# Kernel tuning notes

Measured on AMD Instinct MI355X. Metric: run time of the kernel, lower is better.

## Reference

```python
import jax, jax.numpy as jnp
import numpy as np

D_MODEL = 512
NUM_HEADS = 8
DEPTH = D_MODEL // NUM_HEADS
BATCH = 2
SEQ = 2048
NEG_INF_SCALE = -1e9


def setup_inputs() -> dict:
    key = jax.random.key(0)
    ks = jax.random.split(key, 9)
    s = 0.02
    return {
        "v": jax.random.normal(ks[0], (BATCH, SEQ, D_MODEL), jnp.float32),
        "q": jax.random.normal(ks[1], (BATCH, SEQ, D_MODEL), jnp.float32),
        "k": jax.random.normal(ks[2], (BATCH, SEQ, D_MODEL), jnp.float32),
        "mask": jax.random.randint(ks[3], (BATCH, 1, SEQ, SEQ), 0, 2, jnp.int32),
        "wq_w": jax.random.normal(ks[4], (D_MODEL, D_MODEL), jnp.float32) * s,
        "wq_b": jnp.zeros((D_MODEL,), jnp.float32),
        "wk_w": jax.random.normal(ks[5], (D_MODEL, D_MODEL), jnp.float32) * s,
        "wk_b": jnp.zeros((D_MODEL,), jnp.float32),
        "wv_w": jax.random.normal(ks[6], (D_MODEL, D_MODEL), jnp.float32) * s,
        "wv_b": jnp.zeros((D_MODEL,), jnp.float32),
        "wo_w": jax.random.normal(ks[7], (D_MODEL, D_MODEL), jnp.float32) * s,
        "wo_b": jnp.zeros((D_MODEL,), jnp.float32),
    }


def _split_heads(x, b):
    # [b, s, d_model] -> [b, h, s, depth]
    return x.reshape(b, -1, NUM_HEADS, DEPTH).transpose(0, 2, 1, 3)


def reference(v, q, k, mask, wq_w, wq_b, wk_w, wk_b, wv_w, wv_b, wo_w, wo_b):
    b = q.shape[0]
    vv = _split_heads(v @ wv_w + wv_b, b)  # [b,h,s,d]
    kk = _split_heads(k @ wk_w + wk_b, b)
    qq = _split_heads(q @ wq_w + wq_b, b)
    # NOTE: the original code swaps q/k at the helper call site, so logits = K @ Q^T.
    logits = jnp.einsum("bhkd,bhqd->bhkq", kk, qq) / jnp.sqrt(jnp.float32(DEPTH))
    logits = logits + mask.astype(jnp.float32) * NEG_INF_SCALE
    attn = jax.nn.softmax(logits, axis=-1)  # softmax over the query axis (faithful quirk)
    # output = A^T @ V  -> [b,h,q,d]
    out = jnp.einsum("bhkq,bhkd->bhqd", attn, vv)
    concat = out.transpose(0, 2, 1, 3).reshape(b, -1, D_MODEL)
    return concat @ wo_w + wo_b, attn
```

## Files before the change

kernel.cpp:

```cpp
#include <hip/hip_runtime.h>

#define S 2048
#define DM 512
#define NH 8
#define HD 64
#define NB 2
#define BH (NB * NH)
#define MROWS (NB * S)
#define QW (S / 32)

typedef __bf16 bf16x8 __attribute__((ext_vector_type(8)));
typedef float f32x4 __attribute__((ext_vector_type(4)));

union FragU {
  uint4 u;
  bf16x8 v;
  unsigned short s[8];
};

__device__ __forceinline__ unsigned short f2bf(float x) {
  unsigned u = __float_as_uint(x);
  u += 0x7FFFu + ((u >> 16) & 1u);
  return (unsigned short)(u >> 16);
}

__global__ void k_wtrans(const float* __restrict__ w0, const float* __restrict__ w1,
                         const float* __restrict__ w2, const float* __restrict__ w3,
                         unsigned short* __restrict__ wt) {
  __shared__ float tile[64][65];
  int i = blockIdx.z;
  const float* w = (i == 0) ? w0 : (i == 1) ? w1 : (i == 2) ? w2 : w3;
  int k0 = blockIdx.x * 64;
  int n0 = blockIdx.y * 64;
  int tx = threadIdx.x, ty = threadIdx.y;
  for (int r = ty; r < 64; r += 4)
    tile[r][tx] = w[(size_t)(k0 + r) * DM + n0 + tx];
  __syncthreads();
  unsigned short* o = wt + (size_t)i * DM * DM;
  for (int r = ty; r < 64; r += 4)
    o[(size_t)(n0 + r) * DM + k0 + tx] = f2bf(tile[tx][r]);
}

__global__ __launch_bounds__(256) void k_cvt(
    const float* __restrict__ q, const float* __restrict__ k, const float* __restrict__ v,
    unsigned short* __restrict__ oq, unsigned short* __restrict__ ok, unsigned short* __restrict__ ov) {
  int which = blockIdx.y;
  const float* src = (which == 0) ? q : (which == 1) ? k : v;
  unsigned short* dst = (which == 0) ? oq : (which == 1) ? ok : ov;
  size_t t = (size_t)blockIdx.x * 256 + threadIdx.x;
  const float4* s4 = (const float4*)src + t * 2;
  float4 x = s4[0], y = s4[1];
  FragU f;
  f.s[0] = f2bf(x.x); f.s[1] = f2bf(x.y); f.s[2] = f2bf(x.z); f.s[3] = f2bf(x.w);
  f.s[4] = f2bf(y.x); f.s[5] = f2bf(y.y); f.s[6] = f2bf(y.z); f.s[7] = f2bf(y.w);
  *(uint4*)(dst + t * 8) = f.u;
}

__global__ __launch_bounds__(256) void k_maskpack(const int* __restrict__ mask,
                                                  unsigned* __restrict__ mp) {
  size_t gid = (size_t)blockIdx.x * 256 + threadIdx.x;
  int m = mask[gid];
  unsigned long long bal = __ballot(m != 0);
  int lane = threadIdx.x & 63;
  if (lane == 0) {
    uint2 wds = make_uint2((unsigned)bal, (unsigned)(bal >> 32));
    *(uint2*)&mp[gid >> 5] = wds;
  }
}

__global__ __launch_bounds__(256) void k_proj(
    const unsigned short* __restrict__ inq, const unsigned short* __restrict__ ink,
    const unsigned short* __restrict__ inv, const unsigned short* __restrict__ wt,
    const float* __restrict__ bq, const float* __restrict__ bk, const float* __restrict__ bv,
    unsigned short* __restrict__ oq, unsigned short* __restrict__ ok, unsigned short* __restrict__ ov) {
  int which = blockIdx.z;
  const unsigned short* in = (which == 0) ? inq : (which == 1) ? ink : inv;
  const float* bias = (which == 0) ? bq : (which == 1) ? bk : bv;
  unsigned short* out = (which == 0) ? oq : (which == 1) ? ok : ov;
  const unsigned short* w = wt + (size_t)which * DM * DM;

  int lane = threadIdx.x & 63, wv = threadIdx.x >> 6;
  int m0 = blockIdx.x * 64 + wv * 16;
  int n0 = blockIdx.y * 64;
  int kf = (lane >> 4) * 8;
  int arow = m0 + (lane & 15);

  f32x4 acc[4] = {{0.f, 0.f, 0.f, 0.f}, {0.f, 0.f, 0.f, 0.f},
                  {0.f, 0.f, 0.f, 0.f}, {0.f, 0.f, 0.f, 0.f}};

  for (int kk0 = 0; kk0 < DM; kk0 += 32) {
    FragU af;
    af.u = *(const uint4*)(in + (size_t)arow * DM + kk0 + kf);
#pragma unroll
    for (int nt = 0; nt < 4; nt++) {
      FragU bfr;
      bfr.u = *(const uint4*)(w + (size_t)(n0 + nt * 16 + (lane & 15)) * DM + kk0 + kf);
      acc[nt] = __builtin_amdgcn_mfma_f32_16x16x32_bf16(af.v, bfr.v, acc[nt], 0, 0, 0);
    }
  }
#pragma unroll
  for (int nt = 0; nt < 4; nt++) {
#pragma unroll
    for (int r = 0; r < 4; r++) {
      int row = m0 + (lane >> 4) * 4 + r;
      int col = n0 + nt * 16 + (lane & 15);
      float val = acc[nt][r] + bias[col];
      int b = row >> 11, sIdx = row & (S - 1);
      int h = col >> 6, d = col & 63;
      out[(((size_t)(b * NH + h) * S) + sIdx) * HD + d] = f2bf(val);
    }
  }
}

__global__ void k_vtrans(const unsigned short* __restrict__ vin, unsigned short* __restrict__ vout) {
  __shared__ unsigned short tile[64][65];
  int bh = blockIdx.y;
  int s0 = blockIdx.x * 64;
  int tx = threadIdx.x, ty = threadIdx.y;
  const unsigned short* ip = vin + (size_t)bh * S * HD;
  for (int r = ty; r < 64; r += 4)
    tile[r][tx] = ip[(size_t)(s0 + r) * HD + tx];
  __syncthreads();
  unsigned short* op = vout + (size_t)bh * S * HD;
  for (int r = ty; r < 64; r += 4)
    op[(size_t)r * S + s0 + tx] = tile[tx][r];
}

__global__ __launch_bounds__(256, 4) void k_softmax_z(
    const unsigned short* __restrict__ qq, const unsigned short* __restrict__ kk,
    const unsigned* __restrict__ mp, float* __restrict__ Zsum) {
  int lane = threadIdx.x & 63, w = threadIdx.x >> 6;
  int bh = blockIdx.y;
  int b = bh >> 3;
  int k0 = blockIdx.x * 64 + w * 16;
  int kf = (lane >> 4) * 8;
  int qbase = blockIdx.z * (S / 2);
  int krow_b = k0 + (lane >> 4) * 4;

  const unsigned short* kbase = kk + ((size_t)bh * S + k0 + (lane & 15)) * HD + kf;
  FragU a0, a1;
  a0.u = *(const uint4*)kbase;
  a1.u = *(const uint4*)(kbase + 32);

  const unsigned short* qbaseP = qq + (size_t)bh * S * HD;
  const unsigned* mpb = mp + (size_t)b * S * QW;

  float sum[4] = {0.f, 0.f, 0.f, 0.f};

  for (int q0 = qbase; q0 < qbase + S / 2; q0 += 64) {
    uint2 mw[4];
#pragma unroll
    for (int r = 0; r < 4; r++)
      mw[r] = *(const uint2*)&mpb[(size_t)(krow_b + r) * QW + (q0 >> 5)];
#pragma unroll
    for (int nt = 0; nt < 4; nt++) {
      int qcol = q0 + nt * 16 + (lane & 15);
      const unsigned short* qp = qbaseP + (size_t)qcol * HD + kf;
      FragU b0, b1;
      b0.u = *(const uint4*)qp;
      b1.u = *(const uint4*)(qp + 32);
      f32x4 c = {0.f, 0.f, 0.f, 0.f};
      c = __builtin_amdgcn_mfma_f32_16x16x32_bf16(a0.v, b0.v, c, 0, 0, 0);
      c = __builtin_amdgcn_mfma_f32_16x16x32_bf16(a1.v, b1.v, c, 0, 0, 0);
      unsigned bpos = (unsigned)(nt * 16 + (lane & 15)) & 31u;
#pragma unroll
      for (int r = 0; r < 4; r++) {
        unsigned word = (nt < 2) ? mw[r].x : mw[r].y;
        float e = __expf(c[r] * 0.125f);
        sum[r] += ((word >> bpos) & 1u) ? 0.f : e;
      }
    }
  }
#pragma unroll
  for (int r = 0; r < 4; r++) {
    float s = sum[r];
    s += __shfl_xor(s, 1);
    s += __shfl_xor(s, 2);
    s += __shfl_xor(s, 4);
    s += __shfl_xor(s, 8);
    if ((lane & 15) == 0)
      atomicAdd(&Zsum[(size_t)bh * S + krow_b + r], s);
  }
}

__global__ __launch_bounds__(256) void k_invz(float* __restrict__ z) {
  int t = blockIdx.x * 256 + threadIdx.x;
  z[t] = 1.0f / z[t];
}

__global__ __launch_bounds__(256, 4) void k_attn(
    const unsigned short* __restrict__ qq, const unsigned short* __restrict__ kk,
    const unsigned short* __restrict__ vvT, const unsigned* __restrict__ mp,
    const float* __restrict__ invZ, float* __restrict__ attn_out,
    float* __restrict__ pO) {
  __shared__ __align__(16) unsigned short pT[64][72];
  int lane = threadIdx.x & 63, w = threadIdx.x >> 6;
  int bh = blockIdx.y;
  int b = bh >> 3, h = bh & 7;
  int q0 = blockIdx.x * 64;
  int kbase = blockIdx.z * (S / 2);
  int kf = (lane >> 4) * 8;

  FragU bq[4][2];
#pragma unroll
  for (int nt = 0; nt < 4; nt++) {
    const unsigned short* qp = qq + ((size_t)bh * S + q0 + nt * 16 + (lane & 15)) * HD + kf;
    bq[nt][0].u = *(const uint4*)qp;
    bq[nt][1].u = *(const uint4*)(qp + 32);
  }

  f32x4 o[4] = {{0.f, 0.f, 0.f, 0.f}, {0.f, 0.f, 0.f, 0.f},
                {0.f, 0.f, 0.f, 0.f}, {0.f, 0.f, 0.f, 0.f}};

  const unsigned short* kkb = kk + (size_t)bh * S * HD;
  const unsigned short* vb = vvT + (size_t)bh * HD * S;
  const unsigned* mpb = mp + (size_t)b * S * QW;
  float* ao = attn_out + (size_t)bh * S * S;
  const float* izb = invZ + (size_t)bh * S;
  int q0w = q0 >> 5;

  for (int k0 = kbase; k0 < kbase + S / 2; k0 += 64) {
    int kw = k0 + w * 16;
    int krow_b = kw + (lane >> 4) * 4;
    const unsigned short* kp = kkb + (size_t)(kw + (lane & 15)) * HD + kf;
    FragU a0, a1;
    a0.u = *(const uint4*)kp;
    a1.u = *(const uint4*)(kp + 32);
    float iz[4];
    uint2 mw[4];
#pragma unroll
    for (int r = 0; r < 4; r++) {
      iz[r] = izb[krow_b + r];
      mw[r] = *(const uint2*)&mpb[(size_t)(krow_b + r) * QW + q0w];
    }

#pragma unroll
    for (int nt = 0; nt < 4; nt++) {
      f32x4 c = {0.f, 0.f, 0.f, 0.f};
      c = __builtin_amdgcn_mfma_f32_16x16x32_bf16(a0.v, bq[nt][0].v, c, 0, 0, 0);
      c = __builtin_amdgcn_mfma_f32_16x16x32_bf16(a1.v, bq[nt][1].v, c, 0, 0, 0);
      int ql = nt * 16 + (lane & 15);
      int qcol = q0 + ql;
      unsigned bpos = (unsigned)ql & 31u;
#pragma unroll
      for (int r = 0; r < 4; r++) {
        int kl = w * 16 + (lane >> 4) * 4 + r;
        int krow = k0 + kl;
        unsigned word = (nt < 2) ? mw[r].x : mw[r].y;
        float a = ((word >> bpos) & 1u) ? 0.f : __expf(c[r] * 0.125f) * iz[r];
        ao[(size_t)krow * S + qcol] = a;
        pT[ql][kl] = f2bf(a);
      }
    }
    __syncthreads();

#pragma unroll
    for (int ks = 0; ks < 2; ks++) {
      FragU af;
      af.u = *(const uint4*)(&pT[w * 16 + (lane & 15)][kf + ks * 32]);
#pragma unroll
      for (int nt = 0; nt < 4; nt++) {
        FragU bfr;
        bfr.u = *(const uint4*)(vb + (size_t)(nt * 16 + (lane & 15)) * S + k0 + kf + ks * 32);
        o[nt] = __builtin_amdgcn_mfma_f32_16x16x32_bf16(af.v, bfr.v, o[nt], 0, 0, 0);
      }
    }
    __syncthreads();
  }

  float* pOz = pO + (size_t)blockIdx.z * MROWS * DM;
#pragma unroll
  for (int nt = 0; nt < 4; nt++) {
#pragma unroll
    for (int r = 0; r < 4; r++) {
      int qg = q0 + w * 16 + (lane >> 4) * 4 + r;
      int col = h * 64 + nt * 16 + (lane & 15);
      pOz[((size_t)b * S + qg) * DM + col] = o[nt][r];
    }
  }
}

__global__ __launch_bounds__(256) void k_reduceO(const float* __restrict__ p0,
                                                  const float* __restrict__ p1,
                                                  unsigned short* __restrict__ conc) {
  size_t t = (size_t)blockIdx.x * 256 + threadIdx.x;
  float4 a = ((const float4*)p0)[t];
  float4 b = ((const float4*)p1)[t];
  union { unsigned short s[4]; uint2 u; } o;
  o.s[0] = f2bf(a.x + b.x);
  o.s[1] = f2bf(a.y + b.y);
  o.s[2] = f2bf(a.z + b.z);
  o.s[3] = f2bf(a.w + b.w);
  *(uint2*)(conc + t * 4) = o.u;
}

__global__ __launch_bounds__(256) void k_outproj(
    const unsigned short* __restrict__ concat, const unsigned short* __restrict__ wt,
    const float* __restrict__ bias, float* __restrict__ out) {
  const unsigned short* w = wt + (size_t)3 * DM * DM;
  int lane = threadIdx.x & 63, wv = threadIdx.x >> 6;
  int m0 = blockIdx.x * 64 + wv * 16;
  int n0 = blockIdx.y * 64;
  int kf = (lane >> 4) * 8;

  f32x4 acc[4] = {{0.f, 0.f, 0.f, 0.f}, {0.f, 0.f, 0.f, 0.f},
                  {0.f, 0.f, 0.f, 0.f}, {0.f, 0.f, 0.f, 0.f}};

  for (int kk0 = 0; kk0 < DM; kk0 += 32) {
    FragU af;
    af.u = *(const uint4*)(concat + (size_t)(m0 + (lane & 15)) * DM + kk0 + kf);
#pragma unroll
    for (int nt = 0; nt < 4; nt++) {
      FragU bfr;
      bfr.u = *(const uint4*)(w + (size_t)(n0 + nt * 16 + (lane & 15)) * DM + kk0 + kf);
      acc[nt] = __builtin_amdgcn_mfma_f32_16x16x32_bf16(af.v, bfr.v, acc[nt], 0, 0, 0);
    }
  }
#pragma unroll
  for (int nt = 0; nt < 4; nt++) {
#pragma unroll
    for (int r = 0; r < 4; r++) {
      int row = m0 + (lane >> 4) * 4 + r;
      int col = n0 + nt * 16 + (lane & 15);
      out[(size_t)row * DM + col] = acc[nt][r] + bias[col];
    }
  }
}

extern "C" void kernel_launch(void* const* d_in, const int* in_sizes, int n_in,
                              void* d_out, int out_size, void* d_ws, size_t ws_size,
                              hipStream_t stream) {
  (void)in_sizes; (void)n_in; (void)out_size; (void)ws_size;
  const float* v    = (const float*)d_in[0];
  const float* q    = (const float*)d_in[1];
  const float* k    = (const float*)d_in[2];
  const int*   mask = (const int*)d_in[3];
  const float* wq_w = (const float*)d_in[4];
  const float* wq_b = (const float*)d_in[5];
  const float* wk_w = (const float*)d_in[6];
  const float* wk_b = (const float*)d_in[7];
  const float* wv_w = (const float*)d_in[8];
  const float* wv_b = (const float*)d_in[9];
  const float* wo_w = (const float*)d_in[10];
  const float* wo_b = (const float*)d_in[11];

  char* ws = (char*)d_ws;
  size_t off = 0;
  auto alloc = [&](size_t bytes) {
    char* p = ws + off;
    off += (bytes + 255) & ~(size_t)255;
    return p;
  };
  unsigned short* wt   = (unsigned short*)alloc((size_t)4 * DM * DM * 2);
  unsigned short* qbf  = (unsigned short*)alloc((size_t)MROWS * DM * 2);
  unsigned short* kbf  = (unsigned short*)alloc((size_t)MROWS * DM * 2);
  unsigned short* vbf  = (unsigned short*)alloc((size_t)MROWS * DM * 2);
  unsigned short* qq   = (unsigned short*)alloc((size_t)BH * S * HD * 2);
  unsigned short* kk2  = (unsigned short*)alloc((size_t)BH * S * HD * 2);
  unsigned short* vstd = (unsigned short*)alloc((size_t)BH * S * HD * 2);
  unsigned short* vvT  = (unsigned short*)alloc((size_t)BH * S * HD * 2);
  unsigned*       mp   = (unsigned*)alloc((size_t)NB * S * QW * 4);
  float*          Zs   = (float*)alloc((size_t)BH * S * 4);
  float*          pO   = (float*)alloc((size_t)2 * MROWS * DM * 4);
  unsigned short* conc = (unsigned short*)alloc((size_t)MROWS * DM * 2);

  float* out_final = (float*)d_out;
  float* out_attn  = (float*)d_out + (size_t)MROWS * DM;

  k_wtrans<<<dim3(8, 8, 4), dim3(64, 4), 0, stream>>>(wq_w, wk_w, wv_w, wo_w, wt);
  k_cvt<<<dim3(1024, 3), 256, 0, stream>>>(q, k, v, qbf, kbf, vbf);
  k_maskpack<<<dim3(32768), 256, 0, stream>>>(mask, mp);
  hipMemsetAsync(Zs, 0, (size_t)BH * S * 4, stream);
  k_proj<<<dim3(64, 8, 3), 256, 0, stream>>>(qbf, kbf, vbf, wt, wq_b, wk_b, wv_b, qq, kk2, vstd);
  k_vtrans<<<dim3(32, 16), dim3(64, 4), 0, stream>>>(vstd, vvT);
  k_softmax_z<<<dim3(32, 16, 2), 256, 0, stream>>>(qq, kk2, mp, Zs);
  k_invz<<<dim3(128), 256, 0, stream>>>(Zs);
  k_attn<<<dim3(32, 16, 2), 256, 0, stream>>>(qq, kk2, vvT, mp, Zs, out_attn, pO);
  k_reduceO<<<dim3(2048), 256, 0, stream>>>(pO, pO + (size_t)MROWS * DM, conc);
  k_outproj<<<dim3(64, 8), 256, 0, stream>>>(conc, wt, wo_b, out_final);
}
```

Measured before the change: 576.4 us.

## Fuse prep kernels, fold V transpose into projection, double-buffer P tile

Merges weight transpose, input bf16 conversion, mask bit-packing and the Z-sum zeroing into one launch. The mask packer now builds each 32-bit word per thread from int4 loads instead of a wave ballot. The V projection writes its transposed layout through shared memory directly, which removes the separate transpose kernel and its buffer. The reciprocal kernel is folded into k_attn's per-row loads, and k_attn double-buffers the P tile in LDS so one barrier per iteration can be dropped. This removes several launches and intermediate passes over global memory. The cost is doubled LDS in k_attn and extra divides.

```diff
diff --git a/kernel.cpp b/kernel.cpp
--- a/kernel.cpp
+++ b/kernel.cpp
@@ -24,47 +24,56 @@
   return (unsigned short)(u >> 16);
 }
 
-__global__ void k_wtrans(const float* __restrict__ w0, const float* __restrict__ w1,
-                         const float* __restrict__ w2, const float* __restrict__ w3,
-                         unsigned short* __restrict__ wt) {
+__global__ __launch_bounds__(256) void k_prep(
+    const float* __restrict__ w0, const float* __restrict__ w1,
+    const float* __restrict__ w2, const float* __restrict__ w3,
+    unsigned short* __restrict__ wt,
+    const float* __restrict__ q, const float* __restrict__ k, const float* __restrict__ v,
+    unsigned short* __restrict__ oq, unsigned short* __restrict__ ok, unsigned short* __restrict__ ov,
+    const int* __restrict__ mask, unsigned* __restrict__ mp,
+    float* __restrict__ Zs) {
   __shared__ float tile[64][65];
-  int i = blockIdx.z;
-  const float* w = (i == 0) ? w0 : (i == 1) ? w1 : (i == 2) ? w2 : w3;
-  int k0 = blockIdx.x * 64;
-  int n0 = blockIdx.y * 64;
-  int tx = threadIdx.x, ty = threadIdx.y;
-  for (int r = ty; r < 64; r += 4)
-    tile[r][tx] = w[(size_t)(k0 + r) * DM + n0 + tx];
-  __syncthreads();
-  unsigned short* o = wt + (size_t)i * DM * DM;
-  for (int r = ty; r < 64; r += 4)
-    o[(size_t)(n0 + r) * DM + k0 + tx] = f2bf(tile[tx][r]);
-}
-
-__global__ __launch_bounds__(256) void k_cvt(
-    const float* __restrict__ q, const float* __restrict__ k, const float* __restrict__ v,
-    unsigned short* __restrict__ oq, unsigned short* __restrict__ ok, unsigned short* __restrict__ ov) {
-  int which = blockIdx.y;
-  const float* src = (which == 0) ? q : (which == 1) ? k : v;
-  unsigned short* dst = (which == 0) ? oq : (which == 1) ? ok : ov;
-  size_t t = (size_t)blockIdx.x * 256 + threadIdx.x;
-  const float4* s4 = (const float4*)src + t * 2;
-  float4 x = s4[0], y = s4[1];
-  FragU f;
-  f.s[0] = f2bf(x.x); f.s[1] = f2bf(x.y); f.s[2] = f2bf(x.z); f.s[3] = f2bf(x.w);
-  f.s[4] = f2bf(y.x); f.s[5] = f2bf(y.y); f.s[6] = f2bf(y.z); f.s[7] = f2bf(y.w);
-  *(uint4*)(dst + t * 8) = f.u;
-}
-
-__global__ __launch_bounds__(256) void k_maskpack(const int* __restrict__ mask,
-                                                  unsigned* __restrict__ mp) {
-  size_t gid = (size_t)blockIdx.x * 256 + threadIdx.x;
-  int m = mask[gid];
-  unsigned long long bal = __ballot(m != 0);
-  int lane = threadIdx.x & 63;
-  if (lane == 0) {
-    uint2 wds = make_uint2((unsigned)bal, (unsigned)(bal >> 32));
-    *(uint2*)&mp[gid >> 5] = wds;
+  int bid = blockIdx.x;
+  int tid = threadIdx.x;
+  if (bid < 256) {
+    int i = bid >> 6, rem = bid & 63;
+    const float* w = (i == 0) ? w0 : (i == 1) ? w1 : (i == 2) ? w2 : w3;
+    int k0 = (rem & 7) * 64, n0 = (rem >> 3) * 64;
+    int tx = tid & 63, ty = tid >> 6;
+    for (int r = ty; r < 64; r += 4)
+      tile[r][tx] = w[(size_t)(k0 + r) * DM + n0 + tx];
+    __syncthreads();
+    unsigned short* o = wt + (size_t)i * DM * DM;
+    for (int r = ty; r < 64; r += 4)
+      o[(size_t)(n0 + r) * DM + k0 + tx] = f2bf(tile[tx][r]);
+  } else if (bid < 3328) {
+    int b2 = bid - 256;
+    int which = b2 >> 10;
+    const float* src = (which == 0) ? q : (which == 1) ? k : v;
+    unsigned short* dst = (which == 0) ? oq : (which == 1) ? ok : ov;
+    size_t t = (size_t)(b2 & 1023) * 256 + tid;
+    const float4* s4 = (const float4*)src + t * 2;
+    float4 x = s4[0], y = s4[1];
+    FragU f;
+    f.s[0] = f2bf(x.x); f.s[1] = f2bf(x.y); f.s[2] = f2bf(x.z); f.s[3] = f2bf(x.w);
+    f.s[4] = f2bf(y.x); f.s[5] = f2bf(y.y); f.s[6] = f2bf(y.z); f.s[7] = f2bf(y.w);
+    *(uint4*)(dst + t * 8) = f.u;
+  } else if (bid < 4352) {
+    size_t t = (size_t)(bid - 3328) * 256 + tid;
+    const int4* mb = (const int4*)(mask + t * 32);
+    unsigned bits = 0;
+#pragma unroll
+    for (int c = 0; c < 8; c++) {
+      int4 m = mb[c];
+      bits |= (m.x != 0 ? 1u : 0u) << (c * 4);
+      bits |= (m.y != 0 ? 1u : 0u) << (c * 4 + 1);
+      bits |= (m.z != 0 ? 1u : 0u) << (c * 4 + 2);
+      bits |= (m.w != 0 ? 1u : 0u) << (c * 4 + 3);
+    }
+    mp[t] = bits;
+  } else {
+    int t = (bid - 4352) * 256 + tid;
+    ((float4*)Zs)[t] = make_float4(0.f, 0.f, 0.f, 0.f);
   }
 }
 
@@ -72,11 +81,12 @@
     const unsigned short* __restrict__ inq, const unsigned short* __restrict__ ink,
     const unsigned short* __restrict__ inv, const unsigned short* __restrict__ wt,
     const float* __restrict__ bq, const float* __restrict__ bk, const float* __restrict__ bv,
-    unsigned short* __restrict__ oq, unsigned short* __restrict__ ok, unsigned short* __restrict__ ov) {
+    unsigned short* __restrict__ oq, unsigned short* __restrict__ ok,
+    unsigned short* __restrict__ vvT) {
+  __shared__ __align__(16) unsigned short vt[64][72];
   int which = blockIdx.z;
   const unsigned short* in = (which == 0) ? inq : (which == 1) ? ink : inv;
   const float* bias = (which == 0) ? bq : (which == 1) ? bk : bv;
-  unsigned short* out = (which == 0) ? oq : (which == 1) ? ok : ov;
   const unsigned short* w = wt + (size_t)which * DM * DM;
 
   int lane = threadIdx.x & 63, wv = threadIdx.x >> 6;
@@ -98,32 +108,42 @@
       acc[nt] = __builtin_amdgcn_mfma_f32_16x16x32_bf16(af.v, bfr.v, acc[nt], 0, 0, 0);
     }
   }
-#pragma unroll
-  for (int nt = 0; nt < 4; nt++) {
-#pragma unroll
-    for (int r = 0; r < 4; r++) {
-      int row = m0 + (lane >> 4) * 4 + r;
-      int col = n0 + nt * 16 + (lane & 15);
-      float val = acc[nt][r] + bias[col];
-      int b = row >> 11, sIdx = row & (S - 1);
-      int h = col >> 6, d = col & 63;
-      out[(((size_t)(b * NH + h) * S) + sIdx) * HD + d] = f2bf(val);
-    }
-  }
-}
-
-__global__ void k_vtrans(const unsigned short* __restrict__ vin, unsigned short* __restrict__ vout) {
-  __shared__ unsigned short tile[64][65];
-  int bh = blockIdx.y;
-  int s0 = blockIdx.x * 64;
-  int tx = threadIdx.x, ty = threadIdx.y;
-  const unsigned short* ip = vin + (size_t)bh * S * HD;
-  for (int r = ty; r < 64; r += 4)
-    tile[r][tx] = ip[(size_t)(s0 + r) * HD + tx];
-  __syncthreads();
-  unsigned short* op = vout + (size_t)bh * S * HD;
-  for (int r = ty; r < 64; r += 4)
-    op[(size_t)r * S + s0 + tx] = tile[tx][r];
+
+  if (which < 2) {
+    unsigned short* out = (which == 0) ? oq : ok;
+#pragma unroll
+    for (int nt = 0; nt < 4; nt++) {
+#pragma unroll
+      for (int r = 0; r < 4; r++) {
+        int row = m0 + (lane >> 4) * 4 + r;
+        int col = n0 + nt * 16 + (lane & 15);
+        float val = acc[nt][r] + bias[col];
+        int b = row >> 11, sIdx = row & (S - 1);
+        int h = col >> 6, d = col & 63;
+        out[(((size_t)(b * NH + h) * S) + sIdx) * HD + d] = f2bf(val);
+      }
+    }
+  } else {
+#pragma unroll
+    for (int nt = 0; nt < 4; nt++) {
+#pragma unroll
+      for (int r = 0; r < 4; r++) {
+        int sl = wv * 16 + (lane >> 4) * 4 + r;
+        int dl = nt * 16 + (lane & 15);
+        vt[dl][sl] = f2bf(acc[nt][r] + bias[n0 + dl]);
+      }
+    }
+    __syncthreads();
+    int b = (blockIdx.x * 64) >> 11;
+    int s0l = (blockIdx.x * 64) & (S - 1);
+    int h = n0 >> 6;
+    unsigned short* op = vvT + (size_t)(b * NH + h) * HD * S;
+    int d = threadIdx.x >> 2;
+    int sc = (threadIdx.x & 3) * 16;
+#pragma unroll
+    for (int j = 0; j < 2; j++)
+      *(uint4*)&op[(size_t)d * S + s0l + sc + j * 8] = *(uint4*)&vt[d][sc + j * 8];
+  }
 }
 
 __global__ __launch_bounds__(256, 4) void k_softmax_z(
@@ -183,17 +203,12 @@
   }
 }
 
-__global__ __launch_bounds__(256) void k_invz(float* __restrict__ z) {
-  int t = blockIdx.x * 256 + threadIdx.x;
-  z[t] = 1.0f / z[t];
-}
-
 __global__ __launch_bounds__(256, 4) void k_attn(
     const unsigned short* __restrict__ qq, const unsigned short* __restrict__ kk,
     const unsigned short* __restrict__ vvT, const unsigned* __restrict__ mp,
-    const float* __restrict__ invZ, float* __restrict__ attn_out,
+    const float* __restrict__ Zsum, float* __restrict__ attn_out,
     float* __restrict__ pO) {
-  __shared__ __align__(16) unsigned short pT[64][72];
+  __shared__ __align__(16) unsigned short pT[2][64][72];
   int lane = threadIdx.x & 63, w = threadIdx.x >> 6;
   int bh = blockIdx.y;
   int b = bh >> 3, h = bh & 7;
@@ -216,9 +231,10 @@
   const unsigned short* vb = vvT + (size_t)bh * HD * S;
   const unsigned* mpb = mp + (size_t)b * S * QW;
   float* ao = attn_out + (size_t)bh * S * S;
-  const float* izb = invZ + (size_t)bh * S;
+  const float* zb = Zsum + (size_t)bh * S;
   int q0w = q0 >> 5;
 
+  int buf = 0;
   for (int k0 = kbase; k0 < kbase + S / 2; k0 += 64) {
     int kw = k0 + w * 16;
     int krow_b = kw + (lane >> 4) * 4;
@@ -230,7 +246,7 @@
     uint2 mw[4];
 #pragma unroll
     for (int r = 0; r < 4; r++) {
-      iz[r] = izb[krow_b + r];
+      iz[r] = 1.0f / zb[krow_b + r];
       mw[r] = *(const uint2*)&mpb[(size_t)(krow_b + r) * QW + q0w];
     }
 
@@ -249,15 +265,14 @@
         unsigned word = (nt < 2) ? mw[r].x : mw[r].y;
         float a = ((word >> bpos) & 1u) ? 0.f : __expf(c[r] * 0.125f) * iz[r];
         ao[(size_t)krow * S + qcol] = a;
-        pT[ql][kl] = f2bf(a);
+        pT[buf][ql][kl] = f2bf(a);
       }
     }
     __syncthreads();
-
 #pragma unroll
     for (int ks = 0; ks < 2; ks++) {
       FragU af;
-      af.u = *(const uint4*)(&pT[w * 16 + (lane & 15)][kf + ks * 32]);
+      af.u = *(const uint4*)(&pT[buf][w * 16 + (lane & 15)][kf + ks * 32]);
 #pragma unroll
       for (int nt = 0; nt < 4; nt++) {
         FragU bfr;
@@ -265,7 +280,7 @@
         o[nt] = __builtin_amdgcn_mfma_f32_16x16x32_bf16(af.v, bfr.v, o[nt], 0, 0, 0);
       }
     }
-    __syncthreads();
+    buf ^= 1;
   }
 
   float* pOz = pO + (size_t)blockIdx.z * MROWS * DM;
@@ -357,7 +372,6 @@
   unsigned short* vbf  = (unsigned short*)alloc((size_t)MROWS * DM * 2);
   unsigned short* qq   = (unsigned short*)alloc((size_t)BH * S * HD * 2);
   unsigned short* kk2  = (unsigned short*)alloc((size_t)BH * S * HD * 2);
-  unsigned short* vstd = (unsigned short*)alloc((size_t)BH * S * HD * 2);
   unsigned short* vvT  = (unsigned short*)alloc((size_t)BH * S * HD * 2);
   unsigned*       mp   = (unsigned*)alloc((size_t)NB * S * QW * 4);
   float*          Zs   = (float*)alloc((size_t)BH * S * 4);
@@ -367,14 +381,12 @@
   float* out_final = (float*)d_out;
   float* out_attn  = (float*)d_out + (size_t)MROWS * DM;
 
-  k_wtrans<<<dim3(8, 8, 4), dim3(64, 4), 0, stream>>>(wq_w, wk_w, wv_w, wo_w, wt);
-  k_cvt<<<dim3(1024, 3), 256, 0, stream>>>(q, k, v, qbf, kbf, vbf);
-  k_maskpack<<<dim3(32768), 256, 0, stream>>>(mask, mp);
-  hipMemsetAsync(Zs, 0, (size_t)BH * S * 4, stream);
-  k_proj<<<dim3(64, 8, 3), 256, 0, stream>>>(qbf, kbf, vbf, wt, wq_b, wk_b, wv_b, qq, kk2, vstd);
-  k_vtrans<<<dim3(32, 16), dim3(64, 4), 0, stream>>>(vstd, vvT);
+  k_prep<<<dim3(4384), 256, 0, stream>>>(wq_w, wk_w, wv_w, wo_w, wt,
+                                          q, k, v, qbf, kbf, vbf,
+                                          mask, mp, Zs);
+  k_proj<<<dim3(64, 8, 3), 256, 0, stream>>>(qbf, kbf, vbf, wt, wq_b, wk_b, wv_b,
+                                              qq, kk2, vvT);
   k_softmax_z<<<dim3(32, 16, 2), 256, 0, stream>>>(qq, kk2, mp, Zs);
-  k_invz<<<dim3(128), 256, 0, stream>>>(Zs);
   k_attn<<<dim3(32, 16, 2), 256, 0, stream>>>(qq, kk2, vvT, mp, Zs, out_attn, pO);
   k_reduceO<<<dim3(2048), 256, 0, stream>>>(pO, pO + (size_t)MROWS * DM, conc);
   k_outproj<<<dim3(64, 8), 256, 0, stream>>>(conc, wt, wo_b, out_final);
```

New measurement: 554.6 us. -3.8%, faster.
